# Optimization experiments

Hardware: AMD Instinct MI355X
Metric: run time of the kernel (lower is better)

Reference implementation:

```python
import jax, jax.numpy as jnp
import numpy as np

WS = 8                      # window_size
N = WS * WS                 # 64, Householder dimension
PAD = WS - 1                # reflect-pad total (7)
PAD_LO, PAD_HI = PAD // 2, PAD - PAD // 2  # (3, 4)


def setup_inputs() -> dict:
    key = jax.random.key(0)
    k1, k2 = jax.random.split(key)
    x = jax.random.normal(k1, (2, 8, 256, 256), dtype=jnp.float32)
    v = jax.random.normal(k2, (N, N), dtype=jnp.float32)  # 64 Householder vectors (rows)
    return {"x": x, "v": v}


def _get_A(v):
    # A = prod_i (I - 2 v_i v_i^T / ||v_i||^2), composed left-to-right as in the torch loop.
    # A @ (I - 2 v v^T / s) == A - (2/s) * (A v) v^T  -> rank-1 update per step.
    n = v.shape[-1]
    def step(A, vi):
        s = jnp.sum(vi * vi)
        Av = A @ vi                      # [n]
        return A - (2.0 / s) * jnp.outer(Av, vi), None
    A, _ = jax.lax.scan(step, jnp.eye(n, dtype=v.dtype), v)
    return A


def reference(x, v):
    b, c, H, W = x.shape
    xi = x.reshape(b * c, 1, H, W)
    # reflect padding (3,4) on both spatial dims, as in F.pad(..., mode='reflect')
    xp = jnp.pad(xi, ((0, 0), (0, 0), (PAD_LO, PAD_HI), (PAD_LO, PAD_HI)), mode='reflect')
    # unfold: kernel=8, stride=1, padding=0 -> [bc, 64, H, W] (C=1 so channel ordering matches torch)
    patches = jax.lax.conv_general_dilated_patches(
        xp, filter_shape=(WS, WS), window_strides=(1, 1), padding='VALID')
    cols = patches.reshape(b * c, N, H * W)          # [bc, 64, L]
    A = _get_A(v)                                     # [64, 64]
    # OrthoT1d(dim=1): transpose(1,-1) @ A, transpose back -> out[b,m,l] = sum_k cols[b,k,l] A[k,m]
    out = jnp.einsum('bkl,km->bml', cols, A)          # [bc, 64, L]
    # rearrange 'b (h w) (k1 k2) -> b (h w) k1 k2' with k1=H, k2=W
    return out.reshape(b * c, N, H, W)
```

## Files before the change

### kernel.cpp

```cpp
#include <hip/hip_runtime.h>

#define HSZ 256
#define WSZ 256
#define BC  16
#define NCH 64
#define HW  (HSZ * WSZ)
#define PADLO 3

#define SR 16
#define NTHR 256
#define TR (SR + 7)
#define TC (WSZ + 7)
#define TSTRIDE 272

typedef short bf16x8 __attribute__((ext_vector_type(8)));
typedef float f32x4  __attribute__((ext_vector_type(4)));

__device__ __forceinline__ int reflect_idx(int i) {
    i = (i < 0) ? -i : i;
    i = (i >= HSZ) ? (2 * (HSZ - 1) - i) : i;
    return i;
}

__device__ __forceinline__ unsigned short f2bf(float f) {
    unsigned u = __builtin_bit_cast(unsigned, f);
    u += 0x7FFFu + ((u >> 16) & 1u);
    return (unsigned short)(u >> 16);
}

__global__ void build_A_frags(const float* __restrict__ v,
                              unsigned short* __restrict__ frags) {
    __shared__ float vs[64][64];
    __shared__ float rs[64];
    __shared__ float As[64][64];

    const int t = threadIdx.x;
    const int w = t >> 6;
    const int l = t & 63;
    const int r = (w << 4) | (l & 15);
    const int q = l >> 4;

    for (int idx = t; idx < 64 * 64; idx += NTHR)
        ((float*)vs)[idx] = v[idx];
    __syncthreads();

    if (t < 64) {
        const f32x4* vp = (const f32x4*)vs[t];
        float ss[4] = {0, 0, 0, 0};
#pragma unroll
        for (int c = 0; c < 16; ++c) {
            f32x4 vq = vp[c];
            ss[c & 3] = fmaf(vq[0], vq[0], ss[c & 3]);
            ss[c & 3] = fmaf(vq[1], vq[1], ss[c & 3]);
            ss[c & 3] = fmaf(vq[2], vq[2], ss[c & 3]);
            ss[c & 3] = fmaf(vq[3], vq[3], ss[c & 3]);
        }
        rs[t] = 2.0f / ((ss[0] + ss[1]) + (ss[2] + ss[3]));
    }

    float row[16];
#pragma unroll
    for (int c = 0; c < 16; ++c) row[c] = (q * 16 + c == r) ? 1.0f : 0.0f;

    __syncthreads();

    const f32x4* vq0 = (const f32x4*)&vs[0][q * 16];
    f32x4 nv0 = vq0[0], nv1 = vq0[1], nv2 = vq0[2], nv3 = vq0[3];
    float nrs = rs[0];

    for (int i = 0; i < 64; ++i) {
        f32x4 c0 = nv0, c1 = nv1, c2 = nv2, c3 = nv3;
        const float rcur = nrs;
        if (i < 63) {
            const f32x4* vqn = (const f32x4*)&vs[i + 1][q * 16];
            nv0 = vqn[0]; nv1 = vqn[1]; nv2 = vqn[2]; nv3 = vqn[3];
            nrs = rs[i + 1];
        }
        float vv[16];
#pragma unroll
        for (int j = 0; j < 4; ++j) { vv[j] = c0[j]; vv[4+j] = c1[j]; vv[8+j] = c2[j]; vv[12+j] = c3[j]; }

        float a0 = 0, a1 = 0, a2 = 0, a3 = 0;
#pragma unroll
        for (int c = 0; c < 4; ++c) {
            a0 = fmaf(row[c],      vv[c],      a0);
            a1 = fmaf(row[4 + c],  vv[4 + c],  a1);
            a2 = fmaf(row[8 + c],  vv[8 + c],  a2);
            a3 = fmaf(row[12 + c], vv[12 + c], a3);
        }
        float av = (a0 + a1) + (a2 + a3);
        av += __shfl_xor(av, 16);
        av += __shfl_xor(av, 32);

        const float scale = av * rcur;
#pragma unroll
        for (int c = 0; c < 16; ++c) row[c] = fmaf(-scale, vv[c], row[c]);
    }
#pragma unroll
    for (int c = 0; c < 16; ++c) As[r][q * 16 + c] = row[c];
    __syncthreads();

    const int ln = l & 15, lh = l >> 4;
    const int mb = w;
#pragma unroll
    for (int c2 = 0; c2 < 2; ++c2)
#pragma unroll
        for (int j = 0; j < 8; ++j) {
            float val = As[c2 * 32 + lh * 8 + j][mb * 16 + ln];
            frags[(((mb * 2 + c2) * 64) + l) * 8 + j] = f2bf(val);
        }
}

__global__ __launch_bounds__(256)
void ortho_mfma_plane(const float* __restrict__ x,
                      const unsigned short* __restrict__ frags,
                      float* __restrict__ out) {
    __shared__ float tile[TR][TSTRIDE];

    const int bid = blockIdx.x;
    const int lid = (bid & 7) * 128 + (bid >> 3);
    const int b   = lid >> 6;
    const int rem = lid & 63;
    const int mb  = rem >> 4;
    const int ys  = rem & 15;
    const int y0  = ys * SR;

    const float* __restrict__ xb = x + (size_t)b * HW;

    const int tx = threadIdx.x;
    const int wv = threadIdx.y;
    const int tid = wv * 64 + tx;

    for (int idx = tid; idx < TR * TC; idx += NTHR) {
        const int r = idx / TC;
        const int c = idx - r * TC;
        tile[r][c] = xb[(size_t)reflect_idx(y0 + r - PADLO) * WSZ + reflect_idx(c - PADLO)];
    }

    const int ln = tx & 15, lh = tx >> 4;

    const bf16x8 af0 = *(const bf16x8*)(frags + ((mb * 2 + 0) * 64 + tx) * 8);
    const bf16x8 af1 = *(const bf16x8*)(frags + ((mb * 2 + 1) * 64 + tx) * 8);

    __syncthreads();

    float* __restrict__ outp = out + (size_t)(b * NCH + mb * 16) * HW;

#pragma unroll
    for (int rr = 0; rr < 4; ++rr) {
        const int tyr = wv * 4 + rr;
        const int y   = y0 + tyr;

#pragma unroll
        for (int qq = 0; qq < 4; ++qq) {
            unsigned short bfv[2][16];
#pragma unroll
            for (int c = 0; c < 2; ++c) {
                const f32x4* rp = (const f32x4*)&tile[tyr + 4 * c + lh][64 * qq + 4 * ln];
                f32x4 q0 = rp[0], q1 = rp[1], q2 = rp[2], q3 = rp[3];
                float fl[16];
#pragma unroll
                for (int j = 0; j < 4; ++j) { fl[j] = q0[j]; fl[4+j] = q1[j]; fl[8+j] = q2[j]; fl[12+j] = q3[j]; }
#pragma unroll
                for (int j = 0; j < 16; ++j) bfv[c][j] = f2bf(fl[j]);
            }

            bf16x8 bfrag[2][4];
#pragma unroll
            for (int c = 0; c < 2; ++c)
#pragma unroll
                for (int g = 0; g < 4; ++g)
#pragma unroll
                    for (int j = 0; j < 8; ++j)
                        bfrag[c][g][j] = (short)bfv[c][g + j];

            f32x4 acc[4];
#pragma unroll
            for (int g = 0; g < 4; ++g) {
                acc[g] = (f32x4){0.0f, 0.0f, 0.0f, 0.0f};
                acc[g] = __builtin_amdgcn_mfma_f32_16x16x32_bf16(af0, bfrag[0][g], acc[g], 0, 0, 0);
                acc[g] = __builtin_amdgcn_mfma_f32_16x16x32_bf16(af1, bfrag[1][g], acc[g], 0, 0, 0);
            }

#pragma unroll
            for (int r = 0; r < 4; ++r) {
                const int chl = lh * 4 + r;
                f32x4 vv = { acc[0][r], acc[1][r], acc[2][r], acc[3][r] };
                *(f32x4*)&outp[(size_t)chl * HW + (size_t)y * WSZ + 64 * qq + 4 * ln] = vv;
            }
        }
    }
}

extern "C" void kernel_launch(void* const* d_in, const int* in_sizes, int n_in,
                              void* d_out, int out_size, void* d_ws, size_t ws_size,
                              hipStream_t stream) {
    const float* x = (const float*)d_in[0];
    const float* v = (const float*)d_in[1];
    float* outp = (float*)d_out;
    unsigned short* frags = (unsigned short*)d_ws;

    build_A_frags<<<1, 256, 0, stream>>>(v, frags);

    dim3 grid(BC * 4 * 16);
    dim3 block(64, 4);
    ortho_mfma_plane<<<grid, block, 0, stream>>>(x, frags, outp);
}
```

Baseline: 68.41 us.

## Stage MFMA outputs in LDS for full-row nontemporal stores with smaller row strips

Halves the rows handled per block, which doubles the grid. MFMA results for four rows are now staged in a shared-memory buffer, and each wave then writes whole 1 KB contiguous row segments per channel with nontemporal stores. Before, each store covered only 64-element fragments. The aim is to improve write coalescing and cut cache pollution on the output-bound path. The cost is a 64 KB LDS buffer that limits occupancy, extra syncs, and more redundant halo loads from the smaller strips.

Measured after the change: 69.34 us. No clear change (+1.4%).

```diff
diff --git a/kernel.cpp b/kernel.cpp
--- a/kernel.cpp
+++ b/kernel.cpp
@@ -7,11 +7,12 @@
 #define HW  (HSZ * WSZ)
 #define PADLO 3
 
-#define SR 16
+#define SR 8
 #define NTHR 256
 #define TR (SR + 7)
 #define TC (WSZ + 7)
-#define TSTRIDE 272
+#define TSTRIDE 264
+#define CHP 1024
 
 typedef short bf16x8 __attribute__((ext_vector_type(8)));
 typedef float f32x4  __attribute__((ext_vector_type(4)));
@@ -112,17 +113,18 @@
 }
 
 __global__ __launch_bounds__(256)
-void ortho_mfma_plane(const float* __restrict__ x,
+void ortho_mfma_drain(const float* __restrict__ x,
                       const unsigned short* __restrict__ frags,
                       float* __restrict__ out) {
     __shared__ float tile[TR][TSTRIDE];
+    __shared__ float buf[16 * CHP];
 
     const int bid = blockIdx.x;
-    const int lid = (bid & 7) * 128 + (bid >> 3);
-    const int b   = lid >> 6;
-    const int rem = lid & 63;
-    const int mb  = rem >> 4;
-    const int ys  = rem & 15;
+    const int lid = (bid & 7) * 256 + (bid >> 3);
+    const int b   = lid >> 7;
+    const int rem = lid & 127;
+    const int mb  = rem >> 5;
+    const int ys  = rem & 31;
     const int y0  = ys * SR;
 
     const float* __restrict__ xb = x + (size_t)b * HW;
@@ -144,13 +146,13 @@
 
     __syncthreads();
 
-    float* __restrict__ outp = out + (size_t)(b * NCH + mb * 16) * HW;
-
-#pragma unroll
-    for (int rr = 0; rr < 4; ++rr) {
-        const int tyr = wv * 4 + rr;
-        const int y   = y0 + tyr;
-
+    float* __restrict__ outmb = out + (size_t)(b * NCH + mb * 16) * HW;
+
+#pragma unroll
+    for (int g4 = 0; g4 < 2; ++g4) {
+        const int tyr = g4 * 4 + wv;
+
+        f32x4 acc[4][4];
 #pragma unroll
         for (int qq = 0; qq < 4; ++qq) {
             unsigned short bfv[2][16];
@@ -164,7 +166,6 @@
 #pragma unroll
                 for (int j = 0; j < 16; ++j) bfv[c][j] = f2bf(fl[j]);
             }
-
             bf16x8 bfrag[2][4];
 #pragma unroll
             for (int c = 0; c < 2; ++c)
@@ -174,21 +175,38 @@
                     for (int j = 0; j < 8; ++j)
                         bfrag[c][g][j] = (short)bfv[c][g + j];
 
-            f32x4 acc[4];
 #pragma unroll
             for (int g = 0; g < 4; ++g) {
-                acc[g] = (f32x4){0.0f, 0.0f, 0.0f, 0.0f};
-                acc[g] = __builtin_amdgcn_mfma_f32_16x16x32_bf16(af0, bfrag[0][g], acc[g], 0, 0, 0);
-                acc[g] = __builtin_amdgcn_mfma_f32_16x16x32_bf16(af1, bfrag[1][g], acc[g], 0, 0, 0);
-            }
-
+                acc[qq][g] = (f32x4){0.0f, 0.0f, 0.0f, 0.0f};
+                acc[qq][g] = __builtin_amdgcn_mfma_f32_16x16x32_bf16(af0, bfrag[0][g], acc[qq][g], 0, 0, 0);
+                acc[qq][g] = __builtin_amdgcn_mfma_f32_16x16x32_bf16(af1, bfrag[1][g], acc[qq][g], 0, 0, 0);
+            }
+        }
+
+#pragma unroll
+        for (int qq = 0; qq < 4; ++qq)
 #pragma unroll
             for (int r = 0; r < 4; ++r) {
-                const int chl = lh * 4 + r;
-                f32x4 vv = { acc[0][r], acc[1][r], acc[2][r], acc[3][r] };
-                *(f32x4*)&outp[(size_t)chl * HW + (size_t)y * WSZ + 64 * qq + 4 * ln] = vv;
-            }
-        }
+                f32x4 vv = { acc[qq][0][r], acc[qq][1][r], acc[qq][2][r], acc[qq][3][r] };
+                *(f32x4*)&buf[(lh * 4 + r) * CHP + wv * 256 + 64 * qq + 4 * ln] = vv;
+            }
+
+        __syncthreads();
+
+        const int ybase = y0 + g4 * 4;
+#pragma unroll
+        for (int c = 0; c < 4; ++c) {
+            const int ch = wv * 4 + c;
+            float* __restrict__ outc = outmb + (size_t)ch * HW;
+#pragma unroll
+            for (int row = 0; row < 4; ++row) {
+                f32x4 vv = *(const f32x4*)&buf[ch * CHP + row * 256 + 4 * tx];
+                __builtin_nontemporal_store(
+                    vv, (f32x4*)&outc[(size_t)(ybase + row) * WSZ + 4 * tx]);
+            }
+        }
+
+        if (g4 == 0) __syncthreads();
     }
 }
 
@@ -202,7 +220,7 @@
 
     build_A_frags<<<1, 256, 0, stream>>>(v, frags);
 
-    dim3 grid(BC * 4 * 16);
+    dim3 grid(BC * 4 * (HSZ / SR));
     dim3 block(64, 4);
-    ortho_mfma_plane<<<grid, block, 0, stream>>>(x, frags, outp);
-}
+    ortho_mfma_drain<<<grid, block, 0, stream>>>(x, frags, outp);
+}
```
